# Kernel optimization log

Measured on AMD Instinct MI355X. Metric: run time of the kernel, lower is better.

The kernel has to match this reference:

```python
import jax, jax.numpy as jnp
import numpy as np

NUM_IN, NUM_OUT, SD, BATCH = 2048, 8192, 5, 4096
INIT_DELTA = 0.01


def _dist(a, b):
    # a: [I,1,D], b: [1,O,D] -> [I,O]
    return jnp.sqrt(jnp.sum((a - b) ** 2, axis=-1))


def setup_inputs() -> dict:
    key = jax.random.key(0)
    k1, k2, k3, k4, k5 = jax.random.split(key, 5)
    init_in_pos = jax.random.normal(k1, (NUM_IN, 1, SD), dtype=jnp.float32)
    init_out_pos = jax.random.normal(k2, (1, NUM_OUT, SD), dtype=jnp.float32)
    in_pos = init_in_pos + INIT_DELTA * jax.random.normal(k3, (NUM_IN, 1, SD), dtype=jnp.float32)
    out_pos = init_out_pos + INIT_DELTA * jax.random.normal(k4, (1, NUM_OUT, SD), dtype=jnp.float32)
    inputs = jax.random.normal(k5, (BATCH, NUM_IN), dtype=jnp.float32)
    biases = jnp.zeros((NUM_OUT,), dtype=jnp.float32)
    return {"inputs": inputs, "init_in_pos": init_in_pos, "init_out_pos": init_out_pos,
            "in_pos": in_pos, "out_pos": out_pos, "biases": biases}


def reference(inputs, init_in_pos, init_out_pos, in_pos, out_pos, biases):
    # weight = ||in_pos - out_pos|| - ||init_in_pos - init_out_pos||, shape [I,O]
    w = _dist(in_pos, out_pos) - _dist(init_in_pos, init_out_pos)
    return inputs @ w + biases
```

## Files before the change

### kernel.cpp

```cpp
#include <hip/hip_runtime.h>
#include <hip/hip_bf16.h>
#include <stdint.h>

#define NUM_IN  2048
#define NUM_OUT 8192
#define BATCH   4096
#define SD      5

#define BM 256
#define BN 256
#define BK 64
#define NT (NUM_IN / BK)
#define TILEE (BM * BK)

typedef __bf16 bf16x8 __attribute__((ext_vector_type(8)));
typedef float  f32x4  __attribute__((ext_vector_type(4)));
typedef unsigned short ushort_t;
typedef ushort_t ushort8 __attribute__((ext_vector_type(8)));

static __device__ __forceinline__ ushort_t bf16_bits(float f) {
  __hip_bfloat16 h = __float2bfloat16(f);
  ushort_t u;
  __builtin_memcpy(&u, &h, 2);
  return u;
}

__global__ __launch_bounds__(256) void cvt_kernel(const float* __restrict__ x,
                                                  ushort_t* __restrict__ y) {
  const int i = (blockIdx.x * 256 + threadIdx.x) * 8;
  float4 v0 = *reinterpret_cast<const float4*>(x + i);
  float4 v1 = *reinterpret_cast<const float4*>(x + i + 4);
  ushort8 o;
  o[0] = bf16_bits(v0.x); o[1] = bf16_bits(v0.y);
  o[2] = bf16_bits(v0.z); o[3] = bf16_bits(v0.w);
  o[4] = bf16_bits(v1.x); o[5] = bf16_bits(v1.y);
  o[6] = bf16_bits(v1.z); o[7] = bf16_bits(v1.w);
  *reinterpret_cast<ushort8*>(y + i) = o;
}

__global__ __launch_bounds__(256) void genw_kernel(
    const float* __restrict__ in_pos, const float* __restrict__ out_pos,
    const float* __restrict__ init_in, const float* __restrict__ init_out,
    ushort_t* __restrict__ Wt) {
  __shared__ float s_ip[NUM_IN * SD];
  __shared__ float s_iip[NUM_IN * SD];
  const int tid = threadIdx.x;
#pragma unroll
  for (int i = 0; i < 10; ++i) {
    const int idx = i * 1024 + tid * 4;
    *reinterpret_cast<float4*>(&s_ip[idx]) =
        *reinterpret_cast<const float4*>(in_pos + idx);
    *reinterpret_cast<float4*>(&s_iip[idx]) =
        *reinterpret_cast<const float4*>(init_in + idx);
  }
  __syncthreads();

  const int n  = blockIdx.x * 16 + (tid >> 4);
  const int kg = tid & 15;
  float op[SD], iop[SD];
#pragma unroll
  for (int d = 0; d < SD; ++d) {
    op[d]  = out_pos[n * SD + d];
    iop[d] = init_out[n * SD + d];
  }
#pragma unroll 1
  for (int kb = 0; kb < 16; ++kb) {
    const int k0 = kb * 128 + kg * 8;
    float buf[40], ibuf[40];
#pragma unroll
    for (int j = 0; j < 10; ++j) {
      float4 v = *reinterpret_cast<const float4*>(&s_ip[k0 * SD + j * 4]);
      buf[4 * j + 0] = v.x; buf[4 * j + 1] = v.y;
      buf[4 * j + 2] = v.z; buf[4 * j + 3] = v.w;
      float4 u = *reinterpret_cast<const float4*>(&s_iip[k0 * SD + j * 4]);
      ibuf[4 * j + 0] = u.x; ibuf[4 * j + 1] = u.y;
      ibuf[4 * j + 2] = u.z; ibuf[4 * j + 3] = u.w;
    }
    ushort8 o;
#pragma unroll
    for (int i = 0; i < 8; ++i) {
      float d1 = 0.f, d0 = 0.f;
#pragma unroll
      for (int d = 0; d < SD; ++d) {
        float a = buf[i * SD + d] - op[d];
        float b = ibuf[i * SD + d] - iop[d];
        d1 += a * a;
        d0 += b * b;
      }
      o[i] = bf16_bits(sqrtf(d1) - sqrtf(d0));
    }
    *reinterpret_cast<ushort8*>(Wt + (size_t)n * NUM_IN + k0) = o;
  }
}

__global__ __launch_bounds__(512, 1) void gemm_kernel(
    const ushort_t* __restrict__ A,
    const ushort_t* __restrict__ Bt,
    const float* __restrict__ bias,
    float* __restrict__ C) {
  __shared__ __align__(16) ushort_t sA[2 * TILEE];
  __shared__ __align__(16) ushort_t sB[2 * TILEE];

  const int tid  = threadIdx.x;
  const int w    = tid >> 6;
  const int l    = tid & 63;
  const int wm   = w >> 2;
  const int wn   = w & 3;
  const int lrow = l & 15;
  const int lkc  = l >> 4;

  const int orig = blockIdx.x;
  const int lin  = (orig & 7) * 64 + (orig >> 3);
  const int bx   = lin >> 4;
  const int by   = lin & 15;
  const int m0   = by * BM;
  const int n0   = bx * BN;

  const int ck0 = (lkc ^ (lrow & 7)) * 8;
  const int ck1 = ((4 + lkc) ^ (lrow & 7)) * 8;
  const int Ab  = wm * 4096 + lrow * 64;
  const int Bb  = wn * 2048 + lrow * 64;

  const int d0 = tid, d1 = tid + 512;
  const int lr0 = d0 >> 3, lr1 = d1 >> 3;
  const int c0 = (d0 & 7) ^ (lr0 & 7);
  const int c1 = (d1 & 7) ^ (lr1 & 7);
  const ushort_t* pA0 = A  + (size_t)(m0 + (lr0 >> 6) * 128 + (lr0 & 63)) * NUM_IN + c0 * 8;
  const ushort_t* pA1 = A  + (size_t)(m0 + (lr1 >> 6) * 128 + (lr1 & 63)) * NUM_IN + c1 * 8;
  const ushort_t* pB0 = Bt + (size_t)(n0 + (lr0 >> 5) * 64 + (lr0 & 31)) * NUM_IN + c0 * 8;
  const ushort_t* pB1 = Bt + (size_t)(n0 + (lr1 >> 5) * 64 + (lr1 & 31)) * NUM_IN + c1 * 8;

#define GLDS(src, dst)                                                         \
  __builtin_amdgcn_global_load_lds(                                            \
      reinterpret_cast<const __attribute__((address_space(1))) uint32_t*>(     \
          (uintptr_t)(src)),                                                   \
      reinterpret_cast<__attribute__((address_space(3))) uint32_t*>(           \
          (uintptr_t)(dst)),                                                   \
      16, 0, 0)

#define STAGE_A(bs, mh, kt)                                                    \
  {                                                                            \
    GLDS(pA0 + (size_t)(mh) * 64 * NUM_IN + (kt),                              \
         &sA[(bs) * TILEE + (mh) * 8192 + tid * 8]);                           \
    GLDS(pA1 + (size_t)(mh) * 64 * NUM_IN + (kt),                              \
         &sA[(bs) * TILEE + (mh) * 8192 + tid * 8 + 4096]);                    \
  }
#define STAGE_B(bs, nh, kt)                                                    \
  {                                                                            \
    GLDS(pB0 + (size_t)(nh) * 32 * NUM_IN + (kt),                              \
         &sB[(bs) * TILEE + (nh) * 8192 + tid * 8]);                           \
    GLDS(pB1 + (size_t)(nh) * 32 * NUM_IN + (kt),                              \
         &sB[(bs) * TILEE + (nh) * 8192 + tid * 8 + 4096]);                    \
  }

#define RD_A(arr, bs, mh, ck)                                                  \
  {                                                                            \
    _Pragma("unroll")                                                          \
    for (int mi = 0; mi < 4; ++mi)                                             \
      arr[mi] = *reinterpret_cast<const bf16x8*>(                              \
          &sA[(bs) * TILEE + (mh) * 8192 + Ab + mi * 1024 + (ck)]);            \
  }
#define RD_B(arr, bs, nh, ck)                                                  \
  {                                                                            \
    _Pragma("unroll")                                                          \
    for (int nj = 0; nj < 2; ++nj)                                             \
      arr[nj] = *reinterpret_cast<const bf16x8*>(                              \
          &sB[(bs) * TILEE + (nh) * 8192 + Bb + nj * 1024 + (ck)]);            \
  }

#define MFMA8(mh, nh, Aa, Bb_)                                                 \
  {                                                                            \
    __builtin_amdgcn_s_setprio(1);                                             \
    _Pragma("unroll")                                                          \
    for (int mi = 0; mi < 4; ++mi)                                             \
      _Pragma("unroll")                                                        \
      for (int nj = 0; nj < 2; ++nj)                                           \
        acc[(mh) * 4 + mi][(nh) * 2 + nj] =                                    \
            __builtin_amdgcn_mfma_f32_16x16x32_bf16(                           \
                Aa[mi], Bb_[nj], acc[(mh) * 4 + mi][(nh) * 2 + nj], 0, 0, 0);  \
    __builtin_amdgcn_s_setprio(0);                                             \
  }

#define LGKM(n)  asm volatile("s_waitcnt lgkmcnt(" #n ")" ::: "memory")
#define SCHED0   __builtin_amdgcn_sched_barrier(0)
#define BARRIER  __builtin_amdgcn_s_barrier()
#define VMCNT0   asm volatile("s_waitcnt vmcnt(0)" ::: "memory")

#define KTILE(CUR, NXT, ktn)                                                   \
  {                                                                            \
    STAGE_A(NXT, 0, ktn)                                                       \
    RD_A(aE, CUR, 0, ck0) RD_B(b0, CUR, 0, ck0)                                \
    RD_B(b1, CUR, 1, ck0)                                    \
    LGKM(2); SCHED0;                                                           \
    MFMA8(0, 0, aE, b0)                                                        \
    STAGE_B(NXT, 0, ktn)                                                       \
    RD_A(aO, CUR, 1, ck0)                                    \
    LGKM(4); SCHED0;                                                           \
    MFMA8(0, 1, aE, b1)                                                        \
    STAGE_A(NXT, 1, ktn)                                                       \
    LGKM(0); SCHED0;                                                           \
    MFMA8(1, 0, aO, b0)                                                        \
    STAGE_B(NXT, 1, ktn)                                                       \
    RD_A(aE, CUR, 0, ck1) RD_B(b0, CUR, 0, ck1)              \
    MFMA8(1, 1, aO, b1)                                                        \
    RD_B(b1, CUR, 1, ck1)                                    \
    LGKM(2); SCHED0;                                                           \
    MFMA8(0, 0, aE, b0)                                                        \
    RD_A(aO, CUR, 1, ck1)                                    \
    LGKM(4); SCHED0;                                                           \
    MFMA8(0, 1, aE, b1)                                                        \
    LGKM(0); SCHED0;                                                           \
    MFMA8(1, 0, aO, b0)                                                        \
    MFMA8(1, 1, aO, b1)                                                        \
    VMCNT0;                                                                    \
    BARRIER;                                                                   \
  }

  f32x4 acc[8][4];
#pragma unroll
  for (int i = 0; i < 8; ++i)
#pragma unroll
    for (int j = 0; j < 4; ++j) acc[i][j] = f32x4{0.f, 0.f, 0.f, 0.f};

  bf16x8 aE[4], aO[4], b0[2], b1[2];

  STAGE_A(0, 0, 0) STAGE_B(0, 0, 0) STAGE_A(0, 1, 0) STAGE_B(0, 1, 0)
  VMCNT0;
  BARRIER;

#pragma unroll 1
  for (int tt = 0; tt < NT; tt += 2) {
    const int k1 = (tt + 1) * BK;
    const int k2 = (tt + 2 < NT ? tt + 2 : NT - 1) * BK;
    KTILE(0, 1, k1)
    KTILE(1, 0, k2)
  }

  const int er = l >> 4;
  const int ec = l & 15;
#pragma unroll
  for (int nh = 0; nh < 2; ++nh) {
#pragma unroll
    for (int nj = 0; nj < 2; ++nj) {
      const int col = n0 + wn * 64 + nh * 32 + nj * 16 + ec;
      const float bi = bias[col];
#pragma unroll
      for (int mh = 0; mh < 2; ++mh) {
#pragma unroll
        for (int mi = 0; mi < 4; ++mi) {
#pragma unroll
          for (int j = 0; j < 4; ++j) {
            const int row = m0 + wm * 128 + mh * 64 + mi * 16 + er * 4 + j;
            C[(size_t)row * NUM_OUT + col] =
                acc[mh * 4 + mi][nh * 2 + nj][j] + bi;
          }
        }
      }
    }
  }
#undef KTILE
#undef STAGE_A
#undef STAGE_B
#undef RD_A
#undef RD_B
#undef MFMA8
#undef GLDS
}

extern "C" void kernel_launch(void* const* d_in, const int* in_sizes, int n_in,
                              void* d_out, int out_size, void* d_ws, size_t ws_size,
                              hipStream_t stream) {
  const float* inputs   = (const float*)d_in[0];
  const float* init_in  = (const float*)d_in[1];
  const float* init_out = (const float*)d_in[2];
  const float* in_pos   = (const float*)d_in[3];
  const float* out_pos  = (const float*)d_in[4];
  const float* biases   = (const float*)d_in[5];
  float* out = (float*)d_out;

  ushort_t* Abf = (ushort_t*)d_ws;
  ushort_t* Wt  = (ushort_t*)((char*)d_ws + (size_t)BATCH * NUM_IN * 2);

  cvt_kernel<<<(BATCH * NUM_IN) / (256 * 8), 256, 0, stream>>>(inputs, Abf);
  genw_kernel<<<NUM_OUT / 16, 256, 0, stream>>>(
      in_pos, out_pos, init_in, init_out, Wt);
  gemm_kernel<<<(BATCH / BM) * (NUM_OUT / BN), 512, 0, stream>>>(
      Abf, Wt, biases, out);
}
```

Before: 159.4 us.

## Switch GEMM to BK=32 with four-stage LDS ring and deeper prefetch

Halves the K tile to 32 and keeps four LDS stages in a ring. Loads are issued two tiles ahead and the wait is relaxed from vmcnt(0) to vmcnt(4), so one stage's global loads stay in flight across each barrier. The LDS layout and swizzle are reworked so that two rows share a 64-element line. The aim is to hide global-load latency better, at the cost of twice as many barriers per unit of K and less MFMA work between them.

Result: slower. 169.2 us (+6.1%).

```diff
diff --git a/kernel.cpp b/kernel.cpp
--- a/kernel.cpp
+++ b/kernel.cpp
@@ -9,7 +9,7 @@
 
 #define BM 256
 #define BN 256
-#define BK 64
+#define BK 32
 #define NT (NUM_IN / BK)
 #define TILEE (BM * BK)
 
@@ -98,8 +98,8 @@
     const ushort_t* __restrict__ Bt,
     const float* __restrict__ bias,
     float* __restrict__ C) {
-  __shared__ __align__(16) ushort_t sA[2 * TILEE];
-  __shared__ __align__(16) ushort_t sB[2 * TILEE];
+  __shared__ __align__(16) ushort_t sA[4 * TILEE];
+  __shared__ __align__(16) ushort_t sB[4 * TILEE];
 
   const int tid  = threadIdx.x;
   const int w    = tid >> 6;
@@ -116,19 +116,18 @@
   const int m0   = by * BM;
   const int n0   = bx * BN;
 
-  const int ck0 = (lkc ^ (lrow & 7)) * 8;
-  const int ck1 = ((4 + lkc) ^ (lrow & 7)) * 8;
-  const int Ab  = wm * 4096 + lrow * 64;
-  const int Bb  = wn * 2048 + lrow * 64;
-
-  const int d0 = tid, d1 = tid + 512;
-  const int lr0 = d0 >> 3, lr1 = d1 >> 3;
-  const int c0 = (d0 & 7) ^ (lr0 & 7);
-  const int c1 = (d1 & 7) ^ (lr1 & 7);
-  const ushort_t* pA0 = A  + (size_t)(m0 + (lr0 >> 6) * 128 + (lr0 & 63)) * NUM_IN + c0 * 8;
-  const ushort_t* pA1 = A  + (size_t)(m0 + (lr1 >> 6) * 128 + (lr1 & 63)) * NUM_IN + c1 * 8;
-  const ushort_t* pB0 = Bt + (size_t)(n0 + (lr0 >> 5) * 64 + (lr0 & 31)) * NUM_IN + c0 * 8;
-  const ushort_t* pB1 = Bt + (size_t)(n0 + (lr1 >> 5) * 64 + (lr1 & 31)) * NUM_IN + c1 * 8;
+  const int phys  = ((4 * (lrow & 1) + lkc) ^ (lrow >> 1));
+  const int laneo = (lrow >> 1) * 64 + phys * 8;
+  const int AbW = wm * 4096;
+  const int BbW = wn * 2048;
+
+  const int cc  = (tid & 7) ^ ((tid >> 3) & 7);
+  const int row = 2 * (tid >> 3) + (cc >> 2);
+  const int ke  = (cc & 3) * 8;
+  const ushort_t* pA0 = A  + (size_t)(m0 + row) * NUM_IN + ke;
+  const ushort_t* pA1 = A  + (size_t)(m0 + row + 128) * NUM_IN + ke;
+  const ushort_t* pB0 = Bt + (size_t)(n0 + row) * NUM_IN + ke;
+  const ushort_t* pB1 = Bt + (size_t)(n0 + row + 128) * NUM_IN + ke;
 
 #define GLDS(src, dst)                                                         \
   __builtin_amdgcn_global_load_lds(                                            \
@@ -138,37 +137,30 @@
           (uintptr_t)(dst)),                                                   \
       16, 0, 0)
 
-#define STAGE_A(bs, mh, kt)                                                    \
-  {                                                                            \
-    GLDS(pA0 + (size_t)(mh) * 64 * NUM_IN + (kt),                              \
-         &sA[(bs) * TILEE + (mh) * 8192 + tid * 8]);                           \
-    GLDS(pA1 + (size_t)(mh) * 64 * NUM_IN + (kt),                              \
-         &sA[(bs) * TILEE + (mh) * 8192 + tid * 8 + 4096]);                    \
-  }
-#define STAGE_B(bs, nh, kt)                                                    \
-  {                                                                            \
-    GLDS(pB0 + (size_t)(nh) * 32 * NUM_IN + (kt),                              \
-         &sB[(bs) * TILEE + (nh) * 8192 + tid * 8]);                           \
-    GLDS(pB1 + (size_t)(nh) * 32 * NUM_IN + (kt),                              \
-         &sB[(bs) * TILEE + (nh) * 8192 + tid * 8 + 4096]);                    \
-  }
-
-#define RD_A(arr, bs, mh, ck)                                                  \
+#define STAGE(bs, kt)                                                          \
+  {                                                                            \
+    GLDS(pA0 + (kt), &sA[(bs) * TILEE + tid * 8]);                             \
+    GLDS(pA1 + (kt), &sA[(bs) * TILEE + tid * 8 + 4096]);                      \
+    GLDS(pB0 + (kt), &sB[(bs) * TILEE + tid * 8]);                             \
+    GLDS(pB1 + (kt), &sB[(bs) * TILEE + tid * 8 + 4096]);                      \
+  }
+
+#define RD_A(arr, bs, mh)                                                      \
   {                                                                            \
     _Pragma("unroll")                                                          \
     for (int mi = 0; mi < 4; ++mi)                                             \
       arr[mi] = *reinterpret_cast<const bf16x8*>(                              \
-          &sA[(bs) * TILEE + (mh) * 8192 + Ab + mi * 1024 + (ck)]);            \
-  }
-#define RD_B(arr, bs, nh, ck)                                                  \
+          &sA[(bs) * TILEE + AbW + (mh) * 2048 + mi * 512 + laneo]);           \
+  }
+#define RD_B(arr, bs, nh)                                                      \
   {                                                                            \
     _Pragma("unroll")                                                          \
     for (int nj = 0; nj < 2; ++nj)                                             \
       arr[nj] = *reinterpret_cast<const bf16x8*>(                              \
-          &sB[(bs) * TILEE + (nh) * 8192 + Bb + nj * 1024 + (ck)]);            \
-  }
-
-#define MFMA8(mh, nh, Aa, Bb_)                                                 \
+          &sB[(bs) * TILEE + BbW + (nh) * 1024 + nj * 512 + laneo]);           \
+  }
+
+#define MFMA8(mh, nh, Aa, Bx)                                                  \
   {                                                                            \
     __builtin_amdgcn_s_setprio(1);                                             \
     _Pragma("unroll")                                                          \
@@ -177,42 +169,30 @@
       for (int nj = 0; nj < 2; ++nj)                                           \
         acc[(mh) * 4 + mi][(nh) * 2 + nj] =                                    \
             __builtin_amdgcn_mfma_f32_16x16x32_bf16(                           \
-                Aa[mi], Bb_[nj], acc[(mh) * 4 + mi][(nh) * 2 + nj], 0, 0, 0);  \
+                Aa[mi], Bx[nj], acc[(mh) * 4 + mi][(nh) * 2 + nj], 0, 0, 0);   \
     __builtin_amdgcn_s_setprio(0);                                             \
   }
 
 #define LGKM(n)  asm volatile("s_waitcnt lgkmcnt(" #n ")" ::: "memory")
 #define SCHED0   __builtin_amdgcn_sched_barrier(0)
 #define BARRIER  __builtin_amdgcn_s_barrier()
+#define VMCNT4   asm volatile("s_waitcnt vmcnt(4)" ::: "memory")
 #define VMCNT0   asm volatile("s_waitcnt vmcnt(0)" ::: "memory")
 
 #define KTILE(CUR, NXT, ktn)                                                   \
   {                                                                            \
-    STAGE_A(NXT, 0, ktn)                                                       \
-    RD_A(aE, CUR, 0, ck0) RD_B(b0, CUR, 0, ck0)                                \
-    RD_B(b1, CUR, 1, ck0)                                    \
+    STAGE(NXT, ktn)                                                            \
+    RD_A(aE, CUR, 0) RD_B(b0, CUR, 0)                                          \
+    RD_B(b1, CUR, 1)                                                           \
     LGKM(2); SCHED0;                                                           \
     MFMA8(0, 0, aE, b0)                                                        \
-    STAGE_B(NXT, 0, ktn)                                                       \
-    RD_A(aO, CUR, 1, ck0)                                    \
-    LGKM(4); SCHED0;                                                           \
-    MFMA8(0, 1, aE, b1)                                                        \
-    STAGE_A(NXT, 1, ktn)                                                       \
-    LGKM(0); SCHED0;                                                           \
-    MFMA8(1, 0, aO, b0)                                                        \
-    STAGE_B(NXT, 1, ktn)                                                       \
-    RD_A(aE, CUR, 0, ck1) RD_B(b0, CUR, 0, ck1)              \
-    MFMA8(1, 1, aO, b1)                                                        \
-    RD_B(b1, CUR, 1, ck1)                                    \
-    LGKM(2); SCHED0;                                                           \
-    MFMA8(0, 0, aE, b0)                                                        \
-    RD_A(aO, CUR, 1, ck1)                                    \
+    RD_A(aO, CUR, 1)                                                           \
     LGKM(4); SCHED0;                                                           \
     MFMA8(0, 1, aE, b1)                                                        \
     LGKM(0); SCHED0;                                                           \
     MFMA8(1, 0, aO, b0)                                                        \
     MFMA8(1, 1, aO, b1)                                                        \
-    VMCNT0;                                                                    \
+    VMCNT4;                                                                    \
     BARRIER;                                                                   \
   }
 
@@ -224,16 +204,21 @@
 
   bf16x8 aE[4], aO[4], b0[2], b1[2];
 
-  STAGE_A(0, 0, 0) STAGE_B(0, 0, 0) STAGE_A(0, 1, 0) STAGE_B(0, 1, 0)
-  VMCNT0;
+  STAGE(0, 0)
+  STAGE(1, BK)
+  VMCNT4;
   BARRIER;
 
 #pragma unroll 1
-  for (int tt = 0; tt < NT; tt += 2) {
-    const int k1 = (tt + 1) * BK;
+  for (int tt = 0; tt < NT; tt += 4) {
     const int k2 = (tt + 2 < NT ? tt + 2 : NT - 1) * BK;
-    KTILE(0, 1, k1)
-    KTILE(1, 0, k2)
+    const int k3 = (tt + 3 < NT ? tt + 3 : NT - 1) * BK;
+    const int k4 = (tt + 4 < NT ? tt + 4 : NT - 1) * BK;
+    const int k5 = (tt + 5 < NT ? tt + 5 : NT - 1) * BK;
+    KTILE(0, 2, k2)
+    KTILE(1, 3, k3)
+    KTILE(2, 0, k4)
+    KTILE(3, 1, k5)
   }
 
   const int er = l >> 4;
@@ -259,8 +244,7 @@
     }
   }
 #undef KTILE
-#undef STAGE_A
-#undef STAGE_B
+#undef STAGE
 #undef RD_A
 #undef RD_B
 #undef MFMA8
```
